# Kernel tuning notes

Hardware: AMD Instinct MI355X
Metric: run time of the kernel (lower is better)

Reference implementation:

```python
import jax, jax.numpy as jnp
import numpy as np

B, S, DIM = 1, 2048, 2048
H, KVH = 32, 8
D = DIM // H  # 64


def setup_inputs() -> dict:
    key = jax.random.key(0)
    ks = jax.random.split(key, 10)
    x = jax.random.normal(ks[0], (B, S, DIM), dtype=jnp.float32)
    # RoPE frequencies: theta=10000, per LLaMA
    inv_freq = 1.0 / (10000.0 ** (np.arange(0, D, 2, dtype=np.float32) / D))  # (D/2,)
    angles = np.arange(S, dtype=np.float32)[:, None] * inv_freq[None, :]      # (S, D/2)
    freqs_cos = jnp.asarray(np.cos(angles))
    freqs_sin = jnp.asarray(np.sin(angles))
    # causal mask (1,1,S,S), 1 = keep, 0 = masked
    mask = jnp.tril(jnp.ones((S, S), dtype=jnp.int32))[None, None, :, :]
    w = 0.02
    Wq = jax.random.normal(ks[1], (DIM, H * D), dtype=jnp.float32) * w
    bq = jnp.zeros((H * D,), dtype=jnp.float32)
    Wk = jax.random.normal(ks[2], (DIM, KVH * D), dtype=jnp.float32) * w
    bk = jnp.zeros((KVH * D,), dtype=jnp.float32)
    Wv = jax.random.normal(ks[3], (DIM, KVH * D), dtype=jnp.float32) * w
    bv = jnp.zeros((KVH * D,), dtype=jnp.float32)
    Wo = jax.random.normal(ks[4], (H * D, DIM), dtype=jnp.float32) * w
    bo = jnp.zeros((DIM,), dtype=jnp.float32)
    return {"x": x, "freqs_cos": freqs_cos, "freqs_sin": freqs_sin, "mask": mask,
            "Wq": Wq, "bq": bq, "Wk": Wk, "bk": bk, "Wv": Wv, "bv": bv, "Wo": Wo, "bo": bo}


def _rope(t, cos, sin):
    # t: (B, S, h, D) with D even; rotate consecutive pairs (real form of complex mult)
    tr = t.reshape(*t.shape[:-1], -1, 2)          # (B,S,h,D/2,2)
    c = cos[None, :, None, :]                     # (1,S,1,D/2)
    s = sin[None, :, None, :]
    o0 = tr[..., 0] * c - tr[..., 1] * s
    o1 = tr[..., 0] * s + tr[..., 1] * c
    return jnp.stack([o0, o1], axis=-1).reshape(t.shape)


def reference(x, freqs_cos, freqs_sin, mask, Wq, bq, Wk, bk, Wv, bv, Wo, bo):
    b, s, dim = x.shape
    scale = 1.0 / jnp.sqrt(jnp.asarray(D, dtype=x.dtype))
    q = (x @ Wq + bq).reshape(b, s, H, D)
    k = (x @ Wk + bk).reshape(b, s, KVH, D)
    v = (x @ Wv + bv).reshape(b, s, KVH, D)
    q = _rope(q, freqs_cos, freqs_sin)
    k = _rope(k, freqs_cos, freqs_sin)
    # GQA: repeat kv heads to match query heads
    rep = H // KVH
    k = jnp.repeat(k, rep, axis=2)
    v = jnp.repeat(v, rep, axis=2)
    # to (B, H, S, D)
    q = q.transpose(0, 2, 1, 3)
    k = k.transpose(0, 2, 1, 3)
    v = v.transpose(0, 2, 1, 3)
    scores = jnp.einsum('bhqd,bhkd->bhqk', q, k) * scale   # (B,H,S,S)
    neg = jnp.asarray(jnp.finfo(scores.dtype).min, dtype=scores.dtype)
    scores = jnp.where(mask == 0, neg, scores)
    attn = jax.nn.softmax(scores, axis=-1)
    out = jnp.einsum('bhqk,bhkd->bhqd', attn, v)            # (B,H,S,D)
    out = out.transpose(0, 2, 1, 3).reshape(b, s, H * D)
    return out @ Wo + bo
```

## Files before the change

kernel.cpp:

```cpp
#include <hip/hip_runtime.h>
#include <stdint.h>

#define S_LEN 2048
#define DIM   2048
#define NHEAD 32
#define KVHEAD 8
#define HDIM  64
#define NQKV  3072

typedef __attribute__((ext_vector_type(8))) __bf16 bf16x8;
typedef __attribute__((ext_vector_type(4))) float f32x4;
typedef __attribute__((ext_vector_type(8))) unsigned short u16x8;
typedef __attribute__((ext_vector_type(4))) unsigned int u32x4;

#if __has_builtin(__builtin_amdgcn_exp2f)
#define EXP2F(x) __builtin_amdgcn_exp2f(x)
#else
#define EXP2F(x) exp2f(x)
#endif

__device__ __forceinline__ unsigned short f2bf(float f) {
  unsigned u = __builtin_bit_cast(unsigned, f);
  unsigned r = (u + 0x7FFFu + ((u >> 16) & 1u)) >> 16;
  return (unsigned short)r;
}
__device__ __forceinline__ float bf2f(unsigned short h) {
  unsigned u = ((unsigned)h) << 16;
  return __builtin_bit_cast(float, u);
}

__device__ __forceinline__ void gl_lds16(const void* g, void* l) {
  __builtin_amdgcn_global_load_lds(
      (const __attribute__((address_space(1))) unsigned*)g,
      (__attribute__((address_space(3))) unsigned*)l, 16, 0, 0);
}

__global__ void prep_kernel(const float* __restrict__ x,
                            const float* __restrict__ bq,
                            const float* __restrict__ bk,
                            const float* __restrict__ bv,
                            const float* __restrict__ Wq,
                            const float* __restrict__ Wk,
                            const float* __restrict__ Wv,
                            const float* __restrict__ Wo,
                            unsigned short* __restrict__ xb,
                            unsigned short* __restrict__ WqkvT,
                            unsigned short* __restrict__ WoT,
                            float* __restrict__ bqkv) {
  int idx = blockIdx.x;
  int tid = threadIdx.x;
  if (idx < 10240) {
    __shared__ float t[32][33];
    int bx = idx >> 6, by = idx & 63;
    const float* src; int C, sc, dbase; unsigned short* dst;
    if (bx < 64)      { src = Wq; C = 2048; sc = bx * 32;        dst = WqkvT; dbase = sc; }
    else if (bx < 80) { src = Wk; C = 512;  sc = (bx - 64) * 32; dst = WqkvT; dbase = 2048 + sc; }
    else if (bx < 96) { src = Wv; C = 512;  sc = (bx - 80) * 32; dst = WqkvT; dbase = 2560 + sc; }
    else              { src = Wo; C = 2048; sc = (bx - 96) * 32; dst = WoT;   dbase = sc; }
    int tx = tid & 31, ty = tid >> 5;
#pragma unroll
    for (int j = 0; j < 32; j += 8)
      t[ty + j][tx] = src[(size_t)(by * 32 + ty + j) * C + sc + tx];
    __syncthreads();
#pragma unroll
    for (int j = 0; j < 32; j += 8)
      dst[(size_t)(dbase + ty + j) * 2048 + by * 32 + tx] = f2bf(t[tx][ty + j]);
  } else if (idx < 14336) {
    int i = (idx - 10240) * 256 + tid;
    float4 v = ((const float4*)x)[i];
    ushort4 o;
    o.x = f2bf(v.x); o.y = f2bf(v.y); o.z = f2bf(v.z); o.w = f2bf(v.w);
    ((ushort4*)xb)[i] = o;
  } else {
    int i = (idx - 14336) * 256 + tid;
    if (i < NQKV)
      bqkv[i] = (i < 2048) ? bq[i] : (i < 2560 ? bk[i - 2048] : bv[i - 2560]);
  }
}

__global__ void rope_vt_kernel(unsigned short* __restrict__ qkv,
                               const float* __restrict__ fc,
                               const float* __restrict__ fs,
                               unsigned short* __restrict__ VT) {
  int idx = blockIdx.x;
  int tid = threadIdx.x;
  if (idx < 10240) {
    int i = idx * 256 + tid;
    int row = i / 1280;
    int p   = i - row * 1280;
    int col = (p < 1024) ? (p * 2) : (2048 + (p - 1024) * 2);
    int fi = p & 31;
    float c  = fc[row * 32 + fi];
    float sn = fs[row * 32 + fi];
    unsigned* base = (unsigned*)(qkv + (size_t)row * NQKV + col);
    unsigned v = *base;
    float x0 = bf2f((unsigned short)(v & 0xFFFF));
    float x1 = bf2f((unsigned short)(v >> 16));
    unsigned short o0 = f2bf(x0 * c - x1 * sn);
    unsigned short o1 = f2bf(x0 * sn + x1 * c);
    *base = (unsigned)o0 | ((unsigned)o1 << 16);
  } else {
    __shared__ unsigned short t[32][33];
    int sub = idx - 10240;
    int bx = (sub & 15) * 32;
    int by = (sub >> 4) * 32;
    int tx = tid & 31, ty = tid >> 5;
    const unsigned short* src = qkv + 2560;
#pragma unroll
    for (int j = 0; j < 32; j += 8)
      t[ty + j][tx] = src[(size_t)(by + ty + j) * 3072 + bx + tx];
    __syncthreads();
#pragma unroll
    for (int j = 0; j < 32; j += 8)
      VT[(size_t)(bx + ty + j) * 2048 + by + tx] = t[tx][ty + j];
  }
}

template <int NJ, int OUT_BF16>
__global__ __launch_bounds__(512, 4) void gemm_bt_kernel(
    const unsigned short* __restrict__ A,
    const unsigned short* __restrict__ BT,
    const float* __restrict__ bias,
    void* __restrict__ Cc, int M, int N, int K) {
  constexpr int BUFB = 16384 + NJ * 4096;
  __shared__ char smem[2 * BUFB];
  const int tid = threadIdx.x;
  const int lane = tid & 63;
  const int wid = tid >> 6;
  const int kh = wid >> 2;
  const int wsub = wid & 3;
  const int wm = wsub >> 1, wn = wsub & 1;
  const int rowA0 = blockIdx.x * 128;
  const int rowB0 = blockIdx.y * (32 * NJ);
  const int l15 = lane & 15, l4 = lane >> 4;
  const int kcol = kh * 64 + l4 * 16;

  f32x4 acc[4][NJ];
#pragma unroll
  for (int i = 0; i < 4; i++)
#pragma unroll
    for (int j = 0; j < NJ; j++) acc[i][j] = (f32x4){0.f, 0.f, 0.f, 0.f};

  const int nK = K >> 6;

  auto stage = [&](int buf, int kt) {
    const char* Ab = (const char*)A + ((size_t)rowA0 * K + (size_t)kt * 64) * 2;
    const char* Bb = (const char*)BT + ((size_t)rowB0 * K + (size_t)kt * 64) * 2;
    char* Sb = smem + buf * BUFB;
#pragma unroll
    for (int j = 0; j < 2; ++j) {
      int chunk = wid + 8 * j;
      int o = chunk * 1024 + lane * 16;
      int r = o >> 7;
      int cb = (o & 127) ^ ((r & 7) << 4);
      gl_lds16(Ab + (size_t)r * (K * 2) + cb, Sb + chunk * 1024);
    }
#pragma unroll
    for (int j = 0; j < (NJ + 1) / 2; ++j) {
      int chunk = wid + 8 * j;
      if (chunk < 4 * NJ) {
        int o = chunk * 1024 + lane * 16;
        int r = o >> 7;
        int cb = (o & 127) ^ ((r & 7) << 4);
        gl_lds16(Bb + (size_t)r * (K * 2) + cb, Sb + 16384 + chunk * 1024);
      }
    }
  };

  stage(0, 0);
  __syncthreads();
  int buf = 0;

  for (int kt = 0; kt < nK; ++kt) {
    if (kt + 1 < nK) stage(buf ^ 1, kt + 1);

    bf16x8 af[4], bfr[NJ];
    char* Sb = smem + buf * BUFB;
#pragma unroll
    for (int i = 0; i < 4; i++) {
      int ra = wm * 64 + i * 16 + l15;
      af[i] = *(const bf16x8*)(Sb + ra * 128 + (kcol ^ ((ra & 7) << 4)));
    }
#pragma unroll
    for (int j = 0; j < NJ; j++) {
      int rb = wn * (NJ * 16) + j * 16 + l15;
      bfr[j] = *(const bf16x8*)(Sb + 16384 + rb * 128 + (kcol ^ ((rb & 7) << 4)));
    }
#pragma unroll
    for (int i = 0; i < 4; i++)
#pragma unroll
      for (int j = 0; j < NJ; j++)
        acc[i][j] = __builtin_amdgcn_mfma_f32_16x16x32_bf16(af[i], bfr[j], acc[i][j], 0, 0, 0);
    __syncthreads();
    buf ^= 1;
  }

  f32x4* eps = (f32x4*)smem;
  if (kh == 1) {
#pragma unroll
    for (int i = 0; i < 4; i++)
#pragma unroll
      for (int j = 0; j < NJ; j++)
        eps[wsub * (4 * NJ * 64) + (i * NJ + j) * 64 + lane] = acc[i][j];
  }
  __syncthreads();
  if (kh == 0) {
#pragma unroll
    for (int i = 0; i < 4; i++) {
      int row0 = rowA0 + wm * 64 + i * 16 + l4 * 4;
#pragma unroll
      for (int j = 0; j < NJ; j++) {
        f32x4 oth = eps[wsub * (4 * NJ * 64) + (i * NJ + j) * 64 + lane];
        int col = rowB0 + wn * (NJ * 16) + j * 16 + l15;
        float bv_ = bias[col];
#pragma unroll
        for (int r = 0; r < 4; r++) {
          float v = acc[i][j][r] + oth[r] + bv_;
          size_t idx = (size_t)(row0 + r) * N + col;
          if (OUT_BF16) ((unsigned short*)Cc)[idx] = f2bf(v);
          else          ((float*)Cc)[idx] = v;
        }
      }
    }
  }
}

__global__ __launch_bounds__(512, 4) void attn_kernel(
    const unsigned short* __restrict__ qkv,
    const unsigned short* __restrict__ VT,
    unsigned short* __restrict__ O) {
  __shared__ unsigned short Ks[3][64 * 64];
  __shared__ unsigned short VTs[3][64 * 64];

  const int tid = threadIdx.x;
  const int lane = tid & 63;
  const int w = tid >> 6;
  const int l15 = lane & 15, l4 = lane >> 4;
  const int kvh = blockIdx.x & 7;
  const int qt  = 63 - (blockIdx.x >> 3);
  const int h = kvh * 4 + (w >> 1);
  const int qsub = (w & 1) * 16;
  const int nt = (qt >> 1) + 1;
  const int qbase = qt * 32;

  auto issue = [&](int buf, int t) {
    int kvb = t * 64;
    int o = tid << 4;
    int r = o >> 7;
    int cb = (o & 127) ^ ((r & 7) << 4);
    gl_lds16((const char*)qkv + ((size_t)(kvb + r) * NQKV + 2048 + kvh * 64) * 2 + cb,
             (char*)&Ks[buf][0] + o);
    gl_lds16((const char*)VT + ((size_t)(kvh * 64 + r) * S_LEN + kvb) * 2 + cb,
             (char*)&VTs[buf][0] + o);
  };

  bf16x8 qf[2];
  {
    const unsigned short* qrow = qkv + (size_t)(qbase + qsub + l15) * NQKV + h * 64;
#pragma unroll
    for (int kf = 0; kf < 2; ++kf) {
      u16x8 raw = *(const u16x8*)(qrow + kf * 32 + l4 * 8);
      u16x8 sc;
#pragma unroll
      for (int i = 0; i < 8; i++) sc[i] = f2bf(bf2f(raw[i]) * 0.1803368801111f);
      qf[kf] = __builtin_bit_cast(bf16x8, sc);
    }
  }

  f32x4 oacc[4];
  float lsum = 0.f;
#pragma unroll
  for (int d = 0; d < 4; d++) oacc[d] = (f32x4){0.f, 0.f, 0.f, 0.f};

  issue(0, 0);
  if (nt > 1) issue(1, 1);

  for (int t = 0; t < nt; ++t) {
    if (t + 1 < nt) { asm volatile("s_waitcnt vmcnt(2)" ::: "memory"); }
    else            { asm volatile("s_waitcnt vmcnt(0)" ::: "memory"); }
    __builtin_amdgcn_s_barrier();
    asm volatile("" ::: "memory");
    if (t + 2 < nt) issue((t + 2) % 3, t + 2);
    const int buf = t % 3;

    f32x4 sacc[4];
#pragma unroll
    for (int nf = 0; nf < 4; nf++) sacc[nf] = (f32x4){0.f, 0.f, 0.f, 0.f};
    __builtin_amdgcn_s_setprio(1);
#pragma unroll
    for (int nf = 0; nf < 4; nf++) {
#pragma unroll
      for (int kf = 0; kf < 2; kf++) {
        int row = nf * 16 + l15;
        bf16x8 kb = *(const bf16x8*)((const char*)&Ks[buf][0] + row * 128 +
                                     ((kf * 64 + l4 * 16) ^ ((row & 7) << 4)));
        sacc[nf] = __builtin_amdgcn_mfma_f32_16x16x32_bf16(kb, qf[kf], sacc[nf], 0, 0, 0);
      }
    }
    __builtin_amdgcn_s_setprio(0);

    if (t == nt - 1) {
      int kvb = t * 64;
      int qpos = qbase + qsub + l15;
#pragma unroll
      for (int nf = 0; nf < 4; nf++) {
#pragma unroll
        for (int r = 0; r < 4; r++) {
          int kvpos = kvb + nf * 16 + l4 * 4 + r;
          if (kvpos > qpos) sacc[nf][r] = -3.0e38f;
        }
      }
    }

#pragma unroll
    for (int nf = 0; nf < 4; nf++) {
#pragma unroll
      for (int r = 0; r < 4; r++) {
        float p = EXP2F(sacc[nf][r]);
        lsum += p;
        sacc[nf][r] = p;
      }
    }

    unsigned wds[4][2];
#pragma unroll
    for (int nf = 0; nf < 4; nf++)
#pragma unroll
      for (int m = 0; m < 2; m++)
        asm("v_cvt_pk_bf16_f32 %0, %1, %2"
            : "=v"(wds[nf][m]) : "v"(sacc[nf][2 * m]), "v"(sacc[nf][2 * m + 1]));

    bf16x8 paf[2];
#pragma unroll
    for (int kc = 0; kc < 2; kc++) {
      unsigned a0 = wds[2 * kc][0], b0 = wds[2 * kc + 1][0];
      unsigned a1 = wds[2 * kc][1], b1 = wds[2 * kc + 1][1];
      asm("v_permlane32_swap_b32 %0, %1" : "+v"(a0), "+v"(b0));
      asm("v_permlane16_swap_b32 %0, %1" : "+v"(a0), "+v"(b0));
      asm("v_permlane32_swap_b32 %0, %1" : "+v"(a1), "+v"(b1));
      asm("v_permlane16_swap_b32 %0, %1" : "+v"(a1), "+v"(b1));
      u32x4 afu = (u32x4){a0, a1, b0, b1};
      paf[kc] = __builtin_bit_cast(bf16x8, afu);
    }

    __builtin_amdgcn_s_setprio(1);
#pragma unroll
    for (int kc = 0; kc < 2; kc++) {
#pragma unroll
      for (int df = 0; df < 4; df++) {
        int row = df * 16 + l15;
        bf16x8 vb = *(const bf16x8*)((const char*)&VTs[buf][0] + row * 128 +
                                     ((kc * 64 + l4 * 16) ^ ((row & 7) << 4)));
        oacc[df] = __builtin_amdgcn_mfma_f32_16x16x32_bf16(paf[kc], vb, oacc[df], 0, 0, 0);
      }
    }
    __builtin_amdgcn_s_setprio(0);
  }

  lsum += __shfl_xor(lsum, 16, 64);
  lsum += __shfl_xor(lsum, 32, 64);

#pragma unroll
  for (int r = 0; r < 4; r++) {
    float inv = 1.0f / __shfl(lsum, l4 * 4 + r, 16);
    int qpos = qbase + qsub + l4 * 4 + r;
#pragma unroll
    for (int df = 0; df < 4; df++)
      O[(size_t)qpos * DIM + h * 64 + df * 16 + l15] = f2bf(oacc[df][r] * inv);
  }
}

extern "C" void kernel_launch(void* const* d_in, const int* in_sizes, int n_in,
                              void* d_out, int out_size, void* d_ws, size_t ws_size,
                              hipStream_t stream) {
  const float* x  = (const float*)d_in[0];
  const float* fc = (const float*)d_in[1];
  const float* fs = (const float*)d_in[2];
  const float* Wq = (const float*)d_in[4];
  const float* bq = (const float*)d_in[5];
  const float* Wk = (const float*)d_in[6];
  const float* bk = (const float*)d_in[7];
  const float* Wv = (const float*)d_in[8];
  const float* bv = (const float*)d_in[9];
  const float* Wo = (const float*)d_in[10];
  const float* bo = (const float*)d_in[11];
  float* out = (float*)d_out;

  char* ws = (char*)d_ws;
  unsigned short* xb    = (unsigned short*)(ws + 0);
  unsigned short* WqkvT = (unsigned short*)(ws + 8388608);
  unsigned short* WoT   = (unsigned short*)(ws + 20971520);
  float*          bqkv  = (float*)(ws + 29360128);
  unsigned short* qkv   = (unsigned short*)(ws + 29372416);
  unsigned short* VT    = WqkvT;
  unsigned short* attn  = xb;

  prep_kernel<<<14348, 256, 0, stream>>>(x, bq, bk, bv, Wq, Wk, Wv, Wo,
                                         xb, WqkvT, WoT, bqkv);
  gemm_bt_kernel<3, 1><<<dim3(16, 32), 512, 0, stream>>>(xb, WqkvT, bqkv, qkv, 2048, 3072, 2048);
  rope_vt_kernel<<<11264, 256, 0, stream>>>(qkv, fc, fs, VT);
  attn_kernel<<<512, 512, 0, stream>>>(qkv, VT, attn);
  gemm_bt_kernel<2, 0><<<dim3(16, 32), 512, 0, stream>>>(attn, WoT, bo, out, 2048, 2048, 2048);
}
```

Before: 223.4 us.

## Triple-buffer GEMM loads with vmcnt waits and halve attention block warps

The GEMM switches from a double-buffered loop with two __syncthreads per tile to a three-stage ring that uses s_waitcnt and a single barrier, and fixes the N tile at 64 (the QKV GEMM grid grows to 16x48). The attention kernel drops to 4 waves per block, with each wave handling two 16-row query groups that share the K/V fragment loads, so LDS reads are reused across more MFMAs. This costs extra LDS for the third buffer and more registers per wave, and gives fewer waves per block.

```diff
diff --git a/kernel.cpp b/kernel.cpp
--- a/kernel.cpp
+++ b/kernel.cpp
@@ -116,14 +116,14 @@
   }
 }
 
-template <int NJ, int OUT_BF16>
+template <int OUT_BF16>
 __global__ __launch_bounds__(512, 4) void gemm_bt_kernel(
     const unsigned short* __restrict__ A,
     const unsigned short* __restrict__ BT,
     const float* __restrict__ bias,
     void* __restrict__ Cc, int M, int N, int K) {
-  constexpr int BUFB = 16384 + NJ * 4096;
-  __shared__ char smem[2 * BUFB];
+  constexpr int BUFB = 16384 + 8192;
+  __shared__ char smem[3 * BUFB];
   const int tid = threadIdx.x;
   const int lane = tid & 63;
   const int wid = tid >> 6;
@@ -131,15 +131,15 @@
   const int wsub = wid & 3;
   const int wm = wsub >> 1, wn = wsub & 1;
   const int rowA0 = blockIdx.x * 128;
-  const int rowB0 = blockIdx.y * (32 * NJ);
+  const int rowB0 = blockIdx.y * 64;
   const int l15 = lane & 15, l4 = lane >> 4;
   const int kcol = kh * 64 + l4 * 16;
 
-  f32x4 acc[4][NJ];
+  f32x4 acc[4][2];
 #pragma unroll
   for (int i = 0; i < 4; i++)
 #pragma unroll
-    for (int j = 0; j < NJ; j++) acc[i][j] = (f32x4){0.f, 0.f, 0.f, 0.f};
+    for (int j = 0; j < 2; j++) acc[i][j] = (f32x4){0.f, 0.f, 0.f, 0.f};
 
   const int nK = K >> 6;
 
@@ -148,60 +148,57 @@
     const char* Bb = (const char*)BT + ((size_t)rowB0 * K + (size_t)kt * 64) * 2;
     char* Sb = smem + buf * BUFB;
 #pragma unroll
-    for (int j = 0; j < 2; ++j) {
-      int chunk = wid + 8 * j;
-      int o = chunk * 1024 + lane * 16;
+    for (int h = 0; h < 2; ++h) {
+      int o = h * 8192 + tid * 16;
       int r = o >> 7;
       int cb = (o & 127) ^ ((r & 7) << 4);
-      gl_lds16(Ab + (size_t)r * (K * 2) + cb, Sb + chunk * 1024);
-    }
-#pragma unroll
-    for (int j = 0; j < (NJ + 1) / 2; ++j) {
-      int chunk = wid + 8 * j;
-      if (chunk < 4 * NJ) {
-        int o = chunk * 1024 + lane * 16;
-        int r = o >> 7;
-        int cb = (o & 127) ^ ((r & 7) << 4);
-        gl_lds16(Bb + (size_t)r * (K * 2) + cb, Sb + 16384 + chunk * 1024);
-      }
+      gl_lds16(Ab + (size_t)r * (K * 2) + cb, Sb + o);
+    }
+    {
+      int o = tid * 16;
+      int r = o >> 7;
+      int cb = (o & 127) ^ ((r & 7) << 4);
+      gl_lds16(Bb + (size_t)r * (K * 2) + cb, Sb + 16384 + o);
     }
   };
 
   stage(0, 0);
-  __syncthreads();
-  int buf = 0;
+  if (nK > 1) stage(1, 1);
 
   for (int kt = 0; kt < nK; ++kt) {
-    if (kt + 1 < nK) stage(buf ^ 1, kt + 1);
-
-    bf16x8 af[4], bfr[NJ];
-    char* Sb = smem + buf * BUFB;
+    if (kt + 1 < nK) { asm volatile("s_waitcnt vmcnt(3)" ::: "memory"); }
+    else             { asm volatile("s_waitcnt vmcnt(0)" ::: "memory"); }
+    __builtin_amdgcn_s_barrier();
+    asm volatile("" ::: "memory");
+    if (kt + 2 < nK) stage((kt + 2) % 3, kt + 2);
+    char* Sb = smem + (kt % 3) * BUFB;
+
+    bf16x8 af[4], bfr[2];
 #pragma unroll
     for (int i = 0; i < 4; i++) {
       int ra = wm * 64 + i * 16 + l15;
       af[i] = *(const bf16x8*)(Sb + ra * 128 + (kcol ^ ((ra & 7) << 4)));
     }
 #pragma unroll
-    for (int j = 0; j < NJ; j++) {
-      int rb = wn * (NJ * 16) + j * 16 + l15;
+    for (int j = 0; j < 2; j++) {
+      int rb = wn * 32 + j * 16 + l15;
       bfr[j] = *(const bf16x8*)(Sb + 16384 + rb * 128 + (kcol ^ ((rb & 7) << 4)));
     }
 #pragma unroll
     for (int i = 0; i < 4; i++)
 #pragma unroll
-      for (int j = 0; j < NJ; j++)
+      for (int j = 0; j < 2; j++)
         acc[i][j] = __builtin_amdgcn_mfma_f32_16x16x32_bf16(af[i], bfr[j], acc[i][j], 0, 0, 0);
-    __syncthreads();
-    buf ^= 1;
-  }
-
+  }
+
+  __syncthreads();
   f32x4* eps = (f32x4*)smem;
   if (kh == 1) {
 #pragma unroll
     for (int i = 0; i < 4; i++)
 #pragma unroll
-      for (int j = 0; j < NJ; j++)
-        eps[wsub * (4 * NJ * 64) + (i * NJ + j) * 64 + lane] = acc[i][j];
+      for (int j = 0; j < 2; j++)
+        eps[wsub * 512 + (i * 2 + j) * 64 + lane] = acc[i][j];
   }
   __syncthreads();
   if (kh == 0) {
@@ -209,9 +206,9 @@
     for (int i = 0; i < 4; i++) {
       int row0 = rowA0 + wm * 64 + i * 16 + l4 * 4;
 #pragma unroll
-      for (int j = 0; j < NJ; j++) {
-        f32x4 oth = eps[wsub * (4 * NJ * 64) + (i * NJ + j) * 64 + lane];
-        int col = rowB0 + wn * (NJ * 16) + j * 16 + l15;
+      for (int j = 0; j < 2; j++) {
+        f32x4 oth = eps[wsub * 512 + (i * 2 + j) * 64 + lane];
+        int col = rowB0 + wn * 32 + j * 16 + l15;
         float bv_ = bias[col];
 #pragma unroll
         for (int r = 0; r < 4; r++) {
@@ -225,7 +222,7 @@
   }
 }
 
-__global__ __launch_bounds__(512, 4) void attn_kernel(
+__global__ __launch_bounds__(256, 2) void attn_kernel(
     const unsigned short* __restrict__ qkv,
     const unsigned short* __restrict__ VT,
     unsigned short* __restrict__ O) {
@@ -238,54 +235,61 @@
   const int l15 = lane & 15, l4 = lane >> 4;
   const int kvh = blockIdx.x & 7;
   const int qt  = 63 - (blockIdx.x >> 3);
-  const int h = kvh * 4 + (w >> 1);
-  const int qsub = (w & 1) * 16;
+  const int h = kvh * 4 + w;
   const int nt = (qt >> 1) + 1;
   const int qbase = qt * 32;
 
   auto issue = [&](int buf, int t) {
     int kvb = t * 64;
-    int o = tid << 4;
-    int r = o >> 7;
-    int cb = (o & 127) ^ ((r & 7) << 4);
-    gl_lds16((const char*)qkv + ((size_t)(kvb + r) * NQKV + 2048 + kvh * 64) * 2 + cb,
-             (char*)&Ks[buf][0] + o);
-    gl_lds16((const char*)VT + ((size_t)(kvh * 64 + r) * S_LEN + kvb) * 2 + cb,
-             (char*)&VTs[buf][0] + o);
+#pragma unroll
+    for (int hf = 0; hf < 2; ++hf) {
+      int o = hf * 4096 + tid * 16;
+      int r = o >> 7;
+      int cb = (o & 127) ^ ((r & 7) << 4);
+      gl_lds16((const char*)qkv + ((size_t)(kvb + r) * NQKV + 2048 + kvh * 64) * 2 + cb,
+               (char*)&Ks[buf][0] + o);
+      gl_lds16((const char*)VT + ((size_t)(kvh * 64 + r) * S_LEN + kvb) * 2 + cb,
+               (char*)&VTs[buf][0] + o);
+    }
   };
 
-  bf16x8 qf[2];
-  {
-    const unsigned short* qrow = qkv + (size_t)(qbase + qsub + l15) * NQKV + h * 64;
+  bf16x8 qf[2][2];
+#pragma unroll
+  for (int qg = 0; qg < 2; ++qg) {
+    const unsigned short* qrow = qkv + (size_t)(qbase + qg * 16 + l15) * NQKV + h * 64;
 #pragma unroll
     for (int kf = 0; kf < 2; ++kf) {
       u16x8 raw = *(const u16x8*)(qrow + kf * 32 + l4 * 8);
       u16x8 sc;
 #pragma unroll
       for (int i = 0; i < 8; i++) sc[i] = f2bf(bf2f(raw[i]) * 0.1803368801111f);
-      qf[kf] = __builtin_bit_cast(bf16x8, sc);
-    }
-  }
-
-  f32x4 oacc[4];
-  float lsum = 0.f;
-#pragma unroll
-  for (int d = 0; d < 4; d++) oacc[d] = (f32x4){0.f, 0.f, 0.f, 0.f};
+      qf[qg][kf] = __builtin_bit_cast(bf16x8, sc);
+    }
+  }
+
+  f32x4 oacc[2][4];
+  float lsum[2] = {0.f, 0.f};
+#pragma unroll
+  for (int qg = 0; qg < 2; ++qg)
+#pragma unroll
+    for (int d = 0; d < 4; d++) oacc[qg][d] = (f32x4){0.f, 0.f, 0.f, 0.f};
 
   issue(0, 0);
   if (nt > 1) issue(1, 1);
 
   for (int t = 0; t < nt; ++t) {
-    if (t + 1 < nt) { asm volatile("s_waitcnt vmcnt(2)" ::: "memory"); }
+    if (t + 1 < nt) { asm volatile("s_waitcnt vmcnt(4)" ::: "memory"); }
     else            { asm volatile("s_waitcnt vmcnt(0)" ::: "memory"); }
     __builtin_amdgcn_s_barrier();
     asm volatile("" ::: "memory");
     if (t + 2 < nt) issue((t + 2) % 3, t + 2);
     const int buf = t % 3;
 
-    f32x4 sacc[4];
-#pragma unroll
-    for (int nf = 0; nf < 4; nf++) sacc[nf] = (f32x4){0.f, 0.f, 0.f, 0.f};
+    f32x4 sacc[2][4];
+#pragma unroll
+    for (int qg = 0; qg < 2; ++qg)
+#pragma unroll
+      for (int nf = 0; nf < 4; nf++) sacc[qg][nf] = (f32x4){0.f, 0.f, 0.f, 0.f};
     __builtin_amdgcn_s_setprio(1);
 #pragma unroll
     for (int nf = 0; nf < 4; nf++) {
@@ -294,53 +298,60 @@
         int row = nf * 16 + l15;
         bf16x8 kb = *(const bf16x8*)((const char*)&Ks[buf][0] + row * 128 +
                                      ((kf * 64 + l4 * 16) ^ ((row & 7) << 4)));
-        sacc[nf] = __builtin_amdgcn_mfma_f32_16x16x32_bf16(kb, qf[kf], sacc[nf], 0, 0, 0);
+        sacc[0][nf] = __builtin_amdgcn_mfma_f32_16x16x32_bf16(kb, qf[0][kf], sacc[0][nf], 0, 0, 0);
+        sacc[1][nf] = __builtin_amdgcn_mfma_f32_16x16x32_bf16(kb, qf[1][kf], sacc[1][nf], 0, 0, 0);
       }
     }
     __builtin_amdgcn_s_setprio(0);
 
     if (t == nt - 1) {
       int kvb = t * 64;
-      int qpos = qbase + qsub + l15;
-#pragma unroll
-      for (int nf = 0; nf < 4; nf++) {
-#pragma unroll
-        for (int r = 0; r < 4; r++) {
-          int kvpos = kvb + nf * 16 + l4 * 4 + r;
-          if (kvpos > qpos) sacc[nf][r] = -3.0e38f;
+#pragma unroll
+      for (int qg = 0; qg < 2; ++qg) {
+        int qpos = qbase + qg * 16 + l15;
+#pragma unroll
+        for (int nf = 0; nf < 4; nf++) {
+#pragma unroll
+          for (int r = 0; r < 4; r++) {
+            int kvpos = kvb + nf * 16 + l4 * 4 + r;
+            if (kvpos > qpos) sacc[qg][nf][r] = -3.0e38f;
+          }
         }
       }
     }
 
 #pragma unroll
-    for (int nf = 0; nf < 4; nf++) {
-#pragma unroll
-      for (int r = 0; r < 4; r++) {
-        float p = EXP2F(sacc[nf][r]);
-        lsum += p;
-        sacc[nf][r] = p;
+    for (int qg = 0; qg < 2; ++qg)
+#pragma unroll
+      for (int nf = 0; nf < 4; nf++)
+#pragma unroll
+        for (int r = 0; r < 4; r++) {
+          float p = EXP2F(sacc[qg][nf][r]);
+          lsum[qg] += p;
+          sacc[qg][nf][r] = p;
+        }
+
+    bf16x8 paf[2][2];
+#pragma unroll
+    for (int qg = 0; qg < 2; ++qg) {
+      unsigned wds[4][2];
+#pragma unroll
+      for (int nf = 0; nf < 4; nf++)
+#pragma unroll
+        for (int m = 0; m < 2; m++)
+          asm("v_cvt_pk_bf16_f32 %0, %1, %2"
+              : "=v"(wds[nf][m]) : "v"(sacc[qg][nf][2 * m]), "v"(sacc[qg][nf][2 * m + 1]));
+#pragma unroll
+      for (int kc = 0; kc < 2; kc++) {
+        unsigned a0 = wds[2 * kc][0], b0 = wds[2 * kc + 1][0];
+        unsigned a1 = wds[2 * kc][1], b1 = wds[2 * kc + 1][1];
+        asm("v_permlane32_swap_b32 %0, %1" : "+v"(a0), "+v"(b0));
+        asm("v_permlane16_swap_b32 %0, %1" : "+v"(a0), "+v"(b0));
+        asm("v_permlane32_swap_b32 %0, %1" : "+v"(a1), "+v"(b1));
+        asm("v_permlane16_swap_b32 %0, %1" : "+v"(a1), "+v"(b1));
+        u32x4 afu = (u32x4){a0, a1, b0, b1};
+        paf[qg][kc] = __builtin_bit_cast(bf16x8, afu);
       }
-    }
-
-    unsigned wds[4][2];
-#pragma unroll
-    for (int nf = 0; nf < 4; nf++)
-#pragma unroll
-      for (int m = 0; m < 2; m++)
-        asm("v_cvt_pk_bf16_f32 %0, %1, %2"
-            : "=v"(wds[nf][m]) : "v"(sacc[nf][2 * m]), "v"(sacc[nf][2 * m + 1]));
-
-    bf16x8 paf[2];
-#pragma unroll
-    for (int kc = 0; kc < 2; kc++) {
-      unsigned a0 = wds[2 * kc][0], b0 = wds[2 * kc + 1][0];
-      unsigned a1 = wds[2 * kc][1], b1 = wds[2 * kc + 1][1];
-      asm("v_permlane32_swap_b32 %0, %1" : "+v"(a0), "+v"(b0));
-      asm("v_permlane16_swap_b32 %0, %1" : "+v"(a0), "+v"(b0));
-      asm("v_permlane32_swap_b32 %0, %1" : "+v"(a1), "+v"(b1));
-      asm("v_permlane16_swap_b32 %0, %1" : "+v"(a1), "+v"(b1));
-      u32x4 afu = (u32x4){a0, a1, b0, b1};
-      paf[kc] = __builtin_bit_cast(bf16x8, afu);
     }
 
     __builtin_amdgcn_s_setprio(1);
@@ -351,22 +362,25 @@
         int row = df * 16 + l15;
         bf16x8 vb = *(const bf16x8*)((const char*)&VTs[buf][0] + row * 128 +
                                      ((kc * 64 + l4 * 16) ^ ((row & 7) << 4)));
-        oacc[df] = __builtin_amdgcn_mfma_f32_16x16x32_bf16(paf[kc], vb, oacc[df], 0, 0, 0);
+        oacc[0][df] = __builtin_amdgcn_mfma_f32_16x16x32_bf16(paf[0][kc], vb, oacc[0][df], 0, 0, 0);
+        oacc[1][df] = __builtin_amdgcn_mfma_f32_16x16x32_bf16(paf[1][kc], vb, oacc[1][df], 0, 0, 0);
       }
     }
     __builtin_amdgcn_s_setprio(0);
   }
 
-  lsum += __shfl_xor(lsum, 16, 64);
-  lsum += __shfl_xor(lsum, 32, 64);
-
-#pragma unroll
-  for (int r = 0; r < 4; r++) {
-    float inv = 1.0f / __shfl(lsum, l4 * 4 + r, 16);
-    int qpos = qbase + qsub + l4 * 4 + r;
-#pragma unroll
-    for (int df = 0; df < 4; df++)
-      O[(size_t)qpos * DIM + h * 64 + df * 16 + l15] = f2bf(oacc[df][r] * inv);
+#pragma unroll
+  for (int qg = 0; qg < 2; ++qg) {
+    lsum[qg] += __shfl_xor(lsum[qg], 16, 64);
+    lsum[qg] += __shfl_xor(lsum[qg], 32, 64);
+#pragma unroll
+    for (int r = 0; r < 4; r++) {
+      float inv = 1.0f / __shfl(lsum[qg], l4 * 4 + r, 16);
+      int qpos = qbase + qg * 16 + l4 * 4 + r;
+#pragma unroll
+      for (int df = 0; df < 4; df++)
+        O[(size_t)qpos * DIM + h * 64 + df * 16 + l15] = f2bf(oacc[qg][df][r] * inv);
+    }
   }
 }
 
@@ -397,8 +411,8 @@
 
   prep_kernel<<<14348, 256, 0, stream>>>(x, bq, bk, bv, Wq, Wk, Wv, Wo,
                                          xb, WqkvT, WoT, bqkv);
-  gemm_bt_kernel<3, 1><<<dim3(16, 32), 512, 0, stream>>>(xb, WqkvT, bqkv, qkv, 2048, 3072, 2048);
+  gemm_bt_kernel<1><<<dim3(16, 48), 512, 0, stream>>>(xb, WqkvT, bqkv, qkv, 2048, 3072, 2048);
   rope_vt_kernel<<<11264, 256, 0, stream>>>(qkv, fc, fs, VT);
-  attn_kernel<<<512, 512, 0, stream>>>(qkv, VT, attn);
-  gemm_bt_kernel<2, 0><<<dim3(16, 32), 512, 0, stream>>>(attn, WoT, bo, out, 2048, 2048, 2048);
-}
+  attn_kernel<<<512, 256, 0, stream>>>(qkv, VT, attn);
+  gemm_bt_kernel<0><<<dim3(16, 32), 512, 0, stream>>>(attn, WoT, bo, out, 2048, 2048, 2048);
+}
```

Result: slower. 231.9 us (+3.8%).

## Process two KV tiles per barrier with 4-deep LDS ring; relax GEMM waits

Applied to the files above, without the earlier changes.

The attention kernel moves from a 3-buffer ring with one barrier per KV tile to a 4-buffer ring that processes two tiles per barrier pair. It prefetches four tiles ahead and peels the causal-masked last tile into dedicated remainder paths. The GEMM main loop replaces __syncthreads with an explicit vmcnt wait plus raw s_barrier, so the next stage's loads stay in flight while the current one is consumed. The aim is fewer barriers and deeper load/compute overlap, at the cost of more LDS per block (64KB at 512 threads), which may lower occupancy.

```diff
diff --git a/kernel.cpp b/kernel.cpp
--- a/kernel.cpp
+++ b/kernel.cpp
@@ -168,11 +168,17 @@
   };
 
   stage(0, 0);
-  __syncthreads();
   int buf = 0;
 
   for (int kt = 0; kt < nK; ++kt) {
-    if (kt + 1 < nK) stage(buf ^ 1, kt + 1);
+    if (kt + 1 < nK) {
+      stage(buf ^ 1, kt + 1);
+      asm volatile("s_waitcnt vmcnt(3)" ::: "memory");
+    } else {
+      asm volatile("s_waitcnt vmcnt(0)" ::: "memory");
+    }
+    __builtin_amdgcn_s_barrier();
+    asm volatile("" ::: "memory");
 
     bf16x8 af[4], bfr[NJ];
     char* Sb = smem + buf * BUFB;
@@ -191,7 +197,8 @@
 #pragma unroll
       for (int j = 0; j < NJ; j++)
         acc[i][j] = __builtin_amdgcn_mfma_f32_16x16x32_bf16(af[i], bfr[j], acc[i][j], 0, 0, 0);
-    __syncthreads();
+    __builtin_amdgcn_s_barrier();
+    asm volatile("" ::: "memory");
     buf ^= 1;
   }
 
@@ -229,8 +236,8 @@
     const unsigned short* __restrict__ qkv,
     const unsigned short* __restrict__ VT,
     unsigned short* __restrict__ O) {
-  __shared__ unsigned short Ks[3][64 * 64];
-  __shared__ unsigned short VTs[3][64 * 64];
+  __shared__ unsigned short Ks[4][64 * 64];
+  __shared__ unsigned short VTs[4][64 * 64];
 
   const int tid = threadIdx.x;
   const int lane = tid & 63;
@@ -272,21 +279,10 @@
 #pragma unroll
   for (int d = 0; d < 4; d++) oacc[d] = (f32x4){0.f, 0.f, 0.f, 0.f};
 
-  issue(0, 0);
-  if (nt > 1) issue(1, 1);
-
-  for (int t = 0; t < nt; ++t) {
-    if (t + 1 < nt) { asm volatile("s_waitcnt vmcnt(2)" ::: "memory"); }
-    else            { asm volatile("s_waitcnt vmcnt(0)" ::: "memory"); }
-    __builtin_amdgcn_s_barrier();
-    asm volatile("" ::: "memory");
-    if (t + 2 < nt) issue((t + 2) % 3, t + 2);
-    const int buf = t % 3;
-
+  auto compute_tile = [&](int buf, int kvb, bool domask) {
     f32x4 sacc[4];
 #pragma unroll
     for (int nf = 0; nf < 4; nf++) sacc[nf] = (f32x4){0.f, 0.f, 0.f, 0.f};
-    __builtin_amdgcn_s_setprio(1);
 #pragma unroll
     for (int nf = 0; nf < 4; nf++) {
 #pragma unroll
@@ -297,10 +293,7 @@
         sacc[nf] = __builtin_amdgcn_mfma_f32_16x16x32_bf16(kb, qf[kf], sacc[nf], 0, 0, 0);
       }
     }
-    __builtin_amdgcn_s_setprio(0);
-
-    if (t == nt - 1) {
-      int kvb = t * 64;
+    if (domask) {
       int qpos = qbase + qsub + l15;
 #pragma unroll
       for (int nf = 0; nf < 4; nf++) {
@@ -311,17 +304,14 @@
         }
       }
     }
-
-#pragma unroll
-    for (int nf = 0; nf < 4; nf++) {
+#pragma unroll
+    for (int nf = 0; nf < 4; nf++)
 #pragma unroll
       for (int r = 0; r < 4; r++) {
         float p = EXP2F(sacc[nf][r]);
         lsum += p;
         sacc[nf][r] = p;
       }
-    }
-
     unsigned wds[4][2];
 #pragma unroll
     for (int nf = 0; nf < 4; nf++)
@@ -329,7 +319,6 @@
       for (int m = 0; m < 2; m++)
         asm("v_cvt_pk_bf16_f32 %0, %1, %2"
             : "=v"(wds[nf][m]) : "v"(sacc[nf][2 * m]), "v"(sacc[nf][2 * m + 1]));
-
     bf16x8 paf[2];
 #pragma unroll
     for (int kc = 0; kc < 2; kc++) {
@@ -342,8 +331,6 @@
       u32x4 afu = (u32x4){a0, a1, b0, b1};
       paf[kc] = __builtin_bit_cast(bf16x8, afu);
     }
-
-    __builtin_amdgcn_s_setprio(1);
 #pragma unroll
     for (int kc = 0; kc < 2; kc++) {
 #pragma unroll
@@ -354,7 +341,53 @@
         oacc[df] = __builtin_amdgcn_mfma_f32_16x16x32_bf16(paf[kc], vb, oacc[df], 0, 0, 0);
       }
     }
+  };
+
+  issue(0, 0);
+  if (nt > 1) issue(1, 1);
+  if (nt > 2) issue(2, 2);
+  if (nt > 3) issue(3, 3);
+
+  int t = 0;
+  for (; t + 3 < nt; t += 2) {
+    asm volatile("s_waitcnt vmcnt(4)" ::: "memory");
+    __builtin_amdgcn_s_barrier();
+    asm volatile("" ::: "memory");
+    __builtin_amdgcn_s_setprio(1);
+    compute_tile(t & 3, t * 64, false);
+    compute_tile((t + 1) & 3, (t + 1) * 64, false);
     __builtin_amdgcn_s_setprio(0);
+    __builtin_amdgcn_s_barrier();
+    asm volatile("" ::: "memory");
+    if (t + 4 < nt) issue((t + 4) & 3, t + 4);
+    if (t + 5 < nt) issue((t + 5) & 3, t + 5);
+  }
+  int rem = nt - t;
+  if (rem == 3) {
+    asm volatile("s_waitcnt vmcnt(2)" ::: "memory");
+    __builtin_amdgcn_s_barrier();
+    asm volatile("" ::: "memory");
+    __builtin_amdgcn_s_setprio(1);
+    compute_tile(t & 3, t * 64, false);
+    compute_tile((t + 1) & 3, (t + 1) * 64, false);
+    __builtin_amdgcn_s_setprio(0);
+    asm volatile("s_waitcnt vmcnt(0)" ::: "memory");
+    __builtin_amdgcn_s_barrier();
+    asm volatile("" ::: "memory");
+    compute_tile((t + 2) & 3, (t + 2) * 64, true);
+  } else if (rem == 2) {
+    asm volatile("s_waitcnt vmcnt(0)" ::: "memory");
+    __builtin_amdgcn_s_barrier();
+    asm volatile("" ::: "memory");
+    __builtin_amdgcn_s_setprio(1);
+    compute_tile(t & 3, t * 64, false);
+    compute_tile((t + 1) & 3, (t + 1) * 64, true);
+    __builtin_amdgcn_s_setprio(0);
+  } else {
+    asm volatile("s_waitcnt vmcnt(0)" ::: "memory");
+    __builtin_amdgcn_s_barrier();
+    asm volatile("" ::: "memory");
+    compute_tile(t & 3, t * 64, true);
   }
 
   lsum += __shfl_xor(lsum, 16, 64);
```

New measurement: 215.1 us. -3.7%, faster.
